# Performance work log

Measured on AMD Instinct MI355X. Metric: run time of the kernel, lower is better.

Reference implementation:

```python
import jax, jax.numpy as jnp
import numpy as np

EMBED = 256
HEADS = 8
B, T = 8, 1024


def setup_inputs() -> dict:
    key = jax.random.key(0)
    ks = jax.random.split(key, 6)
    scale = 1.0 / np.sqrt(EMBED)
    embeddings = jax.random.normal(ks[0], (B, T, EMBED), dtype=jnp.float32)
    # per-head full-width projections, stacked: [H, out=EMBED, in=EMBED] (torch Linear layout)
    Wq = jax.random.normal(ks[1], (HEADS, EMBED, EMBED), dtype=jnp.float32) * scale
    Wk = jax.random.normal(ks[2], (HEADS, EMBED, EMBED), dtype=jnp.float32) * scale
    Wv = jax.random.normal(ks[3], (HEADS, EMBED, EMBED), dtype=jnp.float32) * scale
    Wo = jax.random.normal(ks[4], (EMBED, HEADS * EMBED), dtype=jnp.float32) * (1.0 / np.sqrt(HEADS * EMBED))
    bo = jax.random.normal(ks[5], (EMBED,), dtype=jnp.float32) * 0.01
    return {"embeddings": embeddings, "Wq": Wq, "Wk": Wk, "Wv": Wv, "Wo": Wo, "bo": bo}


def reference(embeddings, Wq, Wk, Wv, Wo, bo):
    # x: [b,t,e]; W*: [h, out_e, in_e] (torch Linear: y = x @ W.T)
    q = jnp.einsum('bte,hde->hbtd', embeddings, Wq)
    k = jnp.einsum('bte,hde->hbtd', embeddings, Wk)
    v = jnp.einsum('bte,hde->hbtd', embeddings, Wv)
    # NOTE: original code has no 1/sqrt(d) scaling
    energy = jnp.einsum('hbid,hbjd->hbij', q, k)  # [h,b,t,t]
    t = embeddings.shape[1]
    causal = jnp.triu(jnp.ones((t, t), dtype=bool), k=1)
    energy = jnp.where(causal, -jnp.inf, energy)
    attn = jax.nn.softmax(energy, axis=-1)
    o = jnp.einsum('hbij,hbjd->hbid', attn, v)     # [h,b,t,e]
    b, _, _, e = o.shape[1], o.shape[0], o.shape[2], o.shape[3]
    o = jnp.transpose(o, (1, 2, 0, 3)).reshape(embeddings.shape[0], t, -1)  # [b,t,h*e]
    return o @ Wo.T + bo
```

## Files before the change

kernel.cpp:

```cpp
#include <hip/hip_runtime.h>
#include <hip/hip_bf16.h>

#define EMBED 256
#define HEADS 8
#define BATCH 8
#define SEQ   1024
#define NROWS 8192

typedef __attribute__((ext_vector_type(8))) _Float16 half8;
typedef __attribute__((ext_vector_type(4))) float f32x4;
typedef unsigned int  uint;
typedef unsigned short ushort;

#define QE   ((size_t)2097152)

__device__ __forceinline__ ushort f2h(float f) {
    union { _Float16 h; ushort u; } cv; cv.h = (_Float16)f; return cv.u;
}

__global__ __launch_bounds__(256) void convert_f16(
    const float* __restrict__ X,  const float* __restrict__ Wq,
    const float* __restrict__ Wk, const float* __restrict__ Wv,
    const float* __restrict__ Wo,
    ushort* __restrict__ Xf, ushort* __restrict__ Wqkf,
    ushort* __restrict__ Wvf, ushort* __restrict__ Wof)
{
    const int blk = blockIdx.x;
    const float* src; ushort* dst; int i;
    if (blk < 2048)      { src = X;  dst = Xf;            i = blk * 256 + threadIdx.x; }
    else if (blk < 2560) { src = Wq; dst = Wqkf;          i = (blk - 2048) * 256 + threadIdx.x; }
    else if (blk < 3072) { src = Wk; dst = Wqkf + 524288; i = (blk - 2560) * 256 + threadIdx.x; }
    else if (blk < 3584) { src = Wv; dst = Wvf;           i = (blk - 3072) * 256 + threadIdx.x; }
    else                 { src = Wo; dst = Wof;           i = (blk - 3584) * 256 + threadIdx.x; }
    const float4 v = ((const float4*)src)[i];
    uint2 P;
    P.x = (uint)f2h(v.x) | ((uint)f2h(v.y) << 16);
    P.y = (uint)f2h(v.z) | ((uint)f2h(v.w) << 16);
    ((uint2*)dst)[i] = P;
}

__device__ __forceinline__ void gemm1p_core(
    const ushort* __restrict__ Ag, const ushort* __restrict__ Bg,
    ushort* __restrict__ o0, ushort* __restrict__ o1,
    ushort* Ah, ushort* Bh, int wg, int Ntiles, int mode)
{
    const int m0 = (wg / Ntiles) * 128;
    const int n0 = (wg % Ntiles) * 128;

    const int tid = threadIdx.x, w = tid >> 6, l = tid & 63;
    const int wr = w >> 1, wc = w & 1, g = l >> 4, c16 = l & 15;
    const int sr = l >> 3, sb = l & 7;

    f32x4 acc[4][4];
#pragma unroll
    for (int mi = 0; mi < 4; ++mi)
#pragma unroll
        for (int ni = 0; ni < 4; ++ni) acc[mi][ni] = (f32x4){0.f, 0.f, 0.f, 0.f};

    for (int k0 = 0; k0 < 256; k0 += 64) {
        __syncthreads();
#pragma unroll
        for (int j = 0; j < 4; ++j) {
            const int rb = w * 32 + j * 8;
            const int r  = rb + sr;
            const size_t srcA = (size_t)(m0 + r) * 256 + k0 + ((sb ^ (r & 7)) * 8);
            __builtin_amdgcn_global_load_lds(Ag + srcA, &Ah[rb * 64], 16, 0, 0);
            const size_t srcB = (size_t)(n0 + r) * 256 + k0 + ((sb ^ (r & 7)) * 8);
            __builtin_amdgcn_global_load_lds(Bg + srcB, &Bh[rb * 64], 16, 0, 0);
        }
        asm volatile("s_waitcnt vmcnt(0)" ::: "memory");
        __syncthreads();

#pragma unroll
        for (int kh = 0; kh < 2; ++kh) {
            const int bsel = ((kh << 2) | g) ^ (c16 & 7);
            half8 af[4], bf[4];
#pragma unroll
            for (int mi = 0; mi < 4; ++mi)
                af[mi] = *(const half8*)&Ah[(wr * 64 + mi * 16 + c16) * 64 + bsel * 8];
#pragma unroll
            for (int ni = 0; ni < 4; ++ni)
                bf[ni] = *(const half8*)&Bh[(wc * 64 + ni * 16 + c16) * 64 + bsel * 8];
#pragma unroll
            for (int mi = 0; mi < 4; ++mi)
#pragma unroll
                for (int ni = 0; ni < 4; ++ni)
                    acc[mi][ni] = __builtin_amdgcn_mfma_f32_16x16x32_f16(af[mi], bf[ni], acc[mi][ni], 0, 0, 0);
        }
    }

#pragma unroll
    for (int mi = 0; mi < 4; ++mi)
#pragma unroll
        for (int ni = 0; ni < 4; ++ni) {
            const int n = n0 + wc * 64 + ni * 16 + c16;
            if (mode == 0) {
                const int op = n >> 11, hh = (n >> 8) & 7, d = n & 255;
                ushort* tq = (op ? o1 : o0) + (size_t)hh * QE + d;
#pragma unroll
                for (int j = 0; j < 4; ++j) {
                    const int m = m0 + wr * 64 + mi * 16 + 4 * g + j;
                    tq[(size_t)m * 256] = f2h(acc[mi][ni][j]);
                }
            } else {
#pragma unroll
                for (int j = 0; j < 4; ++j) {
                    const int m = m0 + wr * 64 + mi * 16 + 4 * g + j;
                    o0[(size_t)m * NROWS + n] = f2h(acc[mi][ni][j]);
                }
            }
        }
}

__global__ __launch_bounds__(256) void gemm_qkvt(
    const ushort* __restrict__ Xf,
    const ushort* __restrict__ Wqkf, const ushort* __restrict__ Wvf,
    ushort* __restrict__ qf, ushort* __restrict__ kf, ushort* __restrict__ vtb)
{
    __shared__ __align__(16) ushort Ah[128 * 64];
    __shared__ __align__(16) ushort Bh[128 * 64];
    const int bid = blockIdx.x;
    if (bid < 2048) {
        const int wg = (bid & 7) * 256 + (bid >> 3);
        gemm1p_core(Xf, Wqkf, qf, kf, Ah, Bh, wg, 32, 0);
    } else {
        const int b2 = bid - 2048;
        const int wg = (b2 & 7) * 128 + (b2 >> 3);
        gemm1p_core(Wvf, Xf, vtb, nullptr, Ah, Bh, wg, 64, 1);
    }
}

__global__ __launch_bounds__(256) void gemm_out_f16(
    const ushort* __restrict__ A, const ushort* __restrict__ Bw,
    const float* __restrict__ bias, float* __restrict__ fo)
{
    __shared__ __align__(16) ushort Ah[128 * 64];
    __shared__ __align__(16) ushort Bh[64 * 64];

    const int cpx = gridDim.x >> 3;
    const int wg  = (blockIdx.x & 7) * cpx + (blockIdx.x >> 3);
    const int m0 = (wg >> 2) * 128;
    const int n0 = (wg & 3) * 64;

    const int tid = threadIdx.x, w = tid >> 6, l = tid & 63;
    const int wr = w >> 1, wc = w & 1, g = l >> 4, c16 = l & 15;
    const int sr = l >> 3, sb = l & 7;

    f32x4 acc[4][2];
#pragma unroll
    for (int mi = 0; mi < 4; ++mi)
#pragma unroll
        for (int ni = 0; ni < 2; ++ni) acc[mi][ni] = (f32x4){0.f, 0.f, 0.f, 0.f};

    for (int k0 = 0; k0 < 2048; k0 += 64) {
        __syncthreads();
#pragma unroll
        for (int j = 0; j < 4; ++j) {
            const int rb = w * 32 + j * 8;
            const int r  = rb + sr;
            const size_t src = (size_t)(m0 + r) * 2048 + k0 + ((sb ^ (r & 7)) * 8);
            __builtin_amdgcn_global_load_lds(A + src, &Ah[rb * 64], 16, 0, 0);
        }
#pragma unroll
        for (int j = 0; j < 2; ++j) {
            const int rb = w * 16 + j * 8;
            const int r  = rb + sr;
            const size_t src = (size_t)(n0 + r) * 2048 + k0 + ((sb ^ (r & 7)) * 8);
            __builtin_amdgcn_global_load_lds(Bw + src, &Bh[rb * 64], 16, 0, 0);
        }
        asm volatile("s_waitcnt vmcnt(0)" ::: "memory");
        __syncthreads();

#pragma unroll
        for (int kh = 0; kh < 2; ++kh) {
            const int bsel = ((kh << 2) | g) ^ (c16 & 7);
            half8 af[4], bf[2];
#pragma unroll
            for (int mi = 0; mi < 4; ++mi)
                af[mi] = *(const half8*)&Ah[(wr * 64 + mi * 16 + c16) * 64 + bsel * 8];
#pragma unroll
            for (int ni = 0; ni < 2; ++ni)
                bf[ni] = *(const half8*)&Bh[(wc * 32 + ni * 16 + c16) * 64 + bsel * 8];
#pragma unroll
            for (int mi = 0; mi < 4; ++mi)
#pragma unroll
                for (int ni = 0; ni < 2; ++ni)
                    acc[mi][ni] = __builtin_amdgcn_mfma_f32_16x16x32_f16(af[mi], bf[ni], acc[mi][ni], 0, 0, 0);
        }
    }

#pragma unroll
    for (int mi = 0; mi < 4; ++mi)
#pragma unroll
        for (int ni = 0; ni < 2; ++ni) {
            const int n = n0 + wc * 32 + ni * 16 + c16;
            const float bb = bias[n];
#pragma unroll
            for (int j = 0; j < 4; ++j) {
                const int m = m0 + wr * 64 + mi * 16 + 4 * g + j;
                fo[(size_t)m * 256 + n] = acc[mi][ni][j] + bb;
            }
        }
}

__global__ __launch_bounds__(256, 3) void flash_mfma(
    const ushort* __restrict__ qf, const ushort* __restrict__ kf,
    const ushort* __restrict__ vt, ushort* __restrict__ ocf)
{
    __shared__ __align__(16) ushort Ks[2][32 * 256];
    __shared__ __align__(16) ushort VTs[256 * 32];
    __shared__ __align__(16) ushort Pls[4][512];

    const int bid = blockIdx.x;
    const int idx = bid >> 3;
    const int hb  = (bid & 7) * 8 + (idx & 7);
    const int qst = 15 - (idx >> 3);
    const int h = hb >> 3, b = hb & 7;

    const int tid = threadIdx.x;
    const int w = tid >> 6, l = tid & 63;
    const int g = l >> 4, c16 = l & 15;
    const size_t qk_base = (size_t)h * QE + (size_t)b * (SEQ * EMBED);
    const size_t vt_base = (size_t)h * QE + (size_t)b * SEQ;

    const int psw = (c16 >> 1) & 3;
    const int rsw = c16 & 7;
    const int qw0 = qst * 64 + w * 16;
    const int q0 = qw0 + c16;

    half8 qfr[8];
    {
        const ushort* qr = qf + qk_base + (size_t)q0 * EMBED + g * 8;
#pragma unroll
        for (int kc = 0; kc < 8; ++kc)
            qfr[kc] = *(const half8*)(qr + kc * 32);
    }

    const ushort* kbase = kf + qk_base;
    const ushort* vbase = vt + vt_base;
    const int krow_l = l >> 5, kblk = l & 31;
    const int vd_l = l >> 2,  vblk = l & 3;
    uint koff[4], voff[4];
#pragma unroll
    for (int j = 0; j < 4; ++j) {
        const int row = 8 * w + 2 * j + krow_l;
        koff[j] = (uint)(row * EMBED + ((kblk ^ (row & 7)) * 8));
        const int d = w * 64 + j * 16 + vd_l;
        const int phi = ((d >> 1) ^ (d >> 3)) & 3;
        voff[j] = (uint)(d * NROWS + ((vblk ^ phi) * 8));
    }

    f32x4 acc[16];
#pragma unroll
    for (int dt = 0; dt < 16; ++dt) acc[dt] = (f32x4){0.f, 0.f, 0.f, 0.f};
    float m_r = -1e30f, l_p = 0.f;

    char* pw = (char*)&Pls[w][0];
    const int nkt = 2 * qst + 2;

#pragma unroll
    for (int j = 0; j < 4; ++j)
        __builtin_amdgcn_global_load_lds(kbase + koff[j], &Ks[0][(8 * w + 2 * j) * 256], 16, 0, 0);
    asm volatile("s_waitcnt vmcnt(0)" ::: "memory");
    __syncthreads();

    for (int kt = 0; kt < nkt; ++kt) {
#pragma unroll
        for (int j = 0; j < 4; ++j)
            __builtin_amdgcn_global_load_lds(vbase + voff[j] + kt * 32,
                                             &VTs[(w * 64 + j * 16) * 32], 16, 0, 0);
        if (kt + 1 < nkt) {
            const ushort* kb = kbase + (size_t)(kt + 1) * (32 * EMBED);
#pragma unroll
            for (int j = 0; j < 4; ++j)
                __builtin_amdgcn_global_load_lds(kb + koff[j],
                                                 &Ks[(kt + 1) & 1][(8 * w + 2 * j) * 256], 16, 0, 0);
        }

        const bool active = (kt * 32 <= qw0 + 15);
        if (active) {
            const ushort* Kb = &Ks[kt & 1][0];
            f32x4 s0 = (f32x4){0.f, 0.f, 0.f, 0.f};
            f32x4 s1 = (f32x4){0.f, 0.f, 0.f, 0.f};
#pragma unroll
            for (int kc = 0; kc < 8; ++kc) {
                const int blk = ((kc * 4 + g) ^ rsw) * 8;
                const half8 a0 = *(const half8*)&Kb[c16 * 256 + blk];
                const half8 a1 = *(const half8*)&Kb[(c16 + 16) * 256 + blk];
                s0 = __builtin_amdgcn_mfma_f32_16x16x32_f16(a0, qfr[kc], s0, 0, 0, 0);
                s1 = __builtin_amdgcn_mfma_f32_16x16x32_f16(a1, qfr[kc], s1, 0, 0, 0);
            }
            const int k0b = kt * 32 + 4 * g;
            float p0[4], p1[4];
            float pm = -1e30f;
#pragma unroll
            for (int r = 0; r < 4; ++r) {
                p0[r] = (k0b + r      > q0) ? -1e30f : s0[r];
                p1[r] = (k0b + 16 + r > q0) ? -1e30f : s1[r];
                pm = fmaxf(pm, fmaxf(p0[r], p1[r]));
            }
            if (__any(pm > m_r + 8.f)) {
                float gm = fmaxf(pm, __shfl_xor(pm, 16));
                gm = fmaxf(gm, __shfl_xor(gm, 32));
                const float mn = fmaxf(m_r, gm);
                const float sc = __expf(m_r - mn);
                l_p *= sc;
#pragma unroll
                for (int dt = 0; dt < 16; ++dt) acc[dt] *= sc;
                m_r = mn;
            }
#pragma unroll
            for (int r = 0; r < 4; ++r) {
                p0[r] = __expf(p0[r] - m_r);
                p1[r] = __expf(p1[r] - m_r);
                l_p += p0[r] + p1[r];
            }
#pragma unroll
            for (int t = 0; t < 2; ++t)
#pragma unroll
                for (int u = 0; u < 2; ++u) {
                    const int kk = 16 * t + 4 * g + 2 * u;
                    const int off = c16 * 64 + (((kk >> 3) ^ psw) * 16) + (kk & 7) * 2;
                    const float lo = t ? p1[2 * u] : p0[2 * u];
                    const float hi = t ? p1[2 * u + 1] : p0[2 * u + 1];
                    *(uint*)(pw + off) = (uint)f2h(lo) | ((uint)f2h(hi) << 16);
                }
        }

        asm volatile("s_waitcnt vmcnt(0)" ::: "memory");
        __syncthreads();

        if (active) {
            const half8 pfrag = *(const half8*)(pw + c16 * 64 + ((g ^ psw) * 16));
#pragma unroll
            for (int dt = 0; dt < 16; ++dt) {
                const int d = dt * 16 + c16;
                const int phi = ((d >> 1) ^ (d >> 3)) & 3;
                const half8 va = *(const half8*)&VTs[d * 32 + ((g ^ phi) * 8)];
                acc[dt] = __builtin_amdgcn_mfma_f32_16x16x32_f16(va, pfrag, acc[dt], 0, 0, 0);
            }
        }
        __syncthreads();
    }

    l_p += __shfl_xor(l_p, 16);
    l_p += __shfl_xor(l_p, 32);
    const float inv = 1.f / l_p;
    ushort* orow = ocf + ((size_t)(b * SEQ) + q0) * (HEADS * EMBED) + h * EMBED;
#pragma unroll
    for (int dt = 0; dt < 16; ++dt) {
        const f32x4 o = acc[dt] * inv;
        uint2 P2;
        P2.x = (uint)f2h(o[0]) | ((uint)f2h(o[1]) << 16);
        P2.y = (uint)f2h(o[2]) | ((uint)f2h(o[3]) << 16);
        *(uint2*)(orow + dt * 16 + 4 * g) = P2;
    }
}

extern "C" void kernel_launch(void* const* d_in, const int* in_sizes, int n_in,
                              void* d_out, int out_size, void* d_ws, size_t ws_size,
                              hipStream_t stream) {
    const float* X  = (const float*)d_in[0];
    const float* Wq = (const float*)d_in[1];
    const float* Wk = (const float*)d_in[2];
    const float* Wv = (const float*)d_in[3];
    const float* Wo = (const float*)d_in[4];
    const float* bo = (const float*)d_in[5];

    ushort* ws16 = (ushort*)d_ws;
    ushort* qf   = ws16;
    ushort* kf   = ws16 +  8 * QE;
    ushort* vtb  = ws16 + 16 * QE;
    ushort* ocf  = ws16 + 24 * QE;
    ushort* ex   = ws16 + 32 * QE;
    ushort* Xf   = ex;
    ushort* Wqkf = ex + 2097152;
    ushort* Wvf  = ex + 2097152 + 1048576;
    ushort* Wof  = ex + 2097152 + 1048576 + 524288;
    float*  out  = (float*)d_out;

    convert_f16<<<4096, 256, 0, stream>>>(X, Wq, Wk, Wv, Wo, Xf, Wqkf, Wvf, Wof);

    gemm_qkvt<<<3072, 256, 0, stream>>>(Xf, Wqkf, Wvf, qf, kf, vtb);

    flash_mfma<<<1024, 256, 0, stream>>>(qf, kf, vtb, ocf);

    gemm_out_f16<<<256, 256, 0, stream>>>(ocf, Wof, bo, out);
}
```

Baseline: 141.4 us.

## Relax flash-attention barriers with partial vmcnt waits and halve out-GEMM M tile

In the attention kernel, __syncthreads is replaced by raw s_barrier plus sched_barrier. The wait before the P·V phase now uses vmcnt(4), so the prefetch of the next K tile can stay in flight while V is consumed, with a full wait moved to the end of the iteration. Separately, the output projection GEMM tile shrinks from 128 to 64 rows and launches 512 blocks instead of 256, to fill more CUs. Relying on vmcnt ordering and dropping the compiler's fence semantics risks LDS hazards if the load ordering assumptions are wrong.

```diff
diff --git a/kernel.cpp b/kernel.cpp
--- a/kernel.cpp
+++ b/kernel.cpp
@@ -134,39 +134,33 @@
     const ushort* __restrict__ A, const ushort* __restrict__ Bw,
     const float* __restrict__ bias, float* __restrict__ fo)
 {
-    __shared__ __align__(16) ushort Ah[128 * 64];
+    __shared__ __align__(16) ushort Ah[64 * 64];
     __shared__ __align__(16) ushort Bh[64 * 64];
 
-    const int cpx = gridDim.x >> 3;
-    const int wg  = (blockIdx.x & 7) * cpx + (blockIdx.x >> 3);
-    const int m0 = (wg >> 2) * 128;
+    const int wg = (blockIdx.x & 7) * 64 + (blockIdx.x >> 3);
+    const int m0 = (wg >> 2) * 64;
     const int n0 = (wg & 3) * 64;
 
     const int tid = threadIdx.x, w = tid >> 6, l = tid & 63;
     const int wr = w >> 1, wc = w & 1, g = l >> 4, c16 = l & 15;
     const int sr = l >> 3, sb = l & 7;
 
-    f32x4 acc[4][2];
-#pragma unroll
-    for (int mi = 0; mi < 4; ++mi)
+    f32x4 acc[2][2];
+#pragma unroll
+    for (int mi = 0; mi < 2; ++mi)
 #pragma unroll
         for (int ni = 0; ni < 2; ++ni) acc[mi][ni] = (f32x4){0.f, 0.f, 0.f, 0.f};
 
     for (int k0 = 0; k0 < 2048; k0 += 64) {
         __syncthreads();
-#pragma unroll
-        for (int j = 0; j < 4; ++j) {
-            const int rb = w * 32 + j * 8;
-            const int r  = rb + sr;
-            const size_t src = (size_t)(m0 + r) * 2048 + k0 + ((sb ^ (r & 7)) * 8);
-            __builtin_amdgcn_global_load_lds(A + src, &Ah[rb * 64], 16, 0, 0);
-        }
 #pragma unroll
         for (int j = 0; j < 2; ++j) {
             const int rb = w * 16 + j * 8;
             const int r  = rb + sr;
-            const size_t src = (size_t)(n0 + r) * 2048 + k0 + ((sb ^ (r & 7)) * 8);
-            __builtin_amdgcn_global_load_lds(Bw + src, &Bh[rb * 64], 16, 0, 0);
+            const size_t srcA = (size_t)(m0 + r) * 2048 + k0 + ((sb ^ (r & 7)) * 8);
+            __builtin_amdgcn_global_load_lds(A + srcA, &Ah[rb * 64], 16, 0, 0);
+            const size_t srcB = (size_t)(n0 + r) * 2048 + k0 + ((sb ^ (r & 7)) * 8);
+            __builtin_amdgcn_global_load_lds(Bw + srcB, &Bh[rb * 64], 16, 0, 0);
         }
         asm volatile("s_waitcnt vmcnt(0)" ::: "memory");
         __syncthreads();
@@ -174,15 +168,15 @@
 #pragma unroll
         for (int kh = 0; kh < 2; ++kh) {
             const int bsel = ((kh << 2) | g) ^ (c16 & 7);
-            half8 af[4], bf[2];
-#pragma unroll
-            for (int mi = 0; mi < 4; ++mi)
-                af[mi] = *(const half8*)&Ah[(wr * 64 + mi * 16 + c16) * 64 + bsel * 8];
+            half8 af[2], bf[2];
+#pragma unroll
+            for (int mi = 0; mi < 2; ++mi)
+                af[mi] = *(const half8*)&Ah[(wr * 32 + mi * 16 + c16) * 64 + bsel * 8];
 #pragma unroll
             for (int ni = 0; ni < 2; ++ni)
                 bf[ni] = *(const half8*)&Bh[(wc * 32 + ni * 16 + c16) * 64 + bsel * 8];
 #pragma unroll
-            for (int mi = 0; mi < 4; ++mi)
+            for (int mi = 0; mi < 2; ++mi)
 #pragma unroll
                 for (int ni = 0; ni < 2; ++ni)
                     acc[mi][ni] = __builtin_amdgcn_mfma_f32_16x16x32_f16(af[mi], bf[ni], acc[mi][ni], 0, 0, 0);
@@ -190,14 +184,14 @@
     }
 
 #pragma unroll
-    for (int mi = 0; mi < 4; ++mi)
+    for (int mi = 0; mi < 2; ++mi)
 #pragma unroll
         for (int ni = 0; ni < 2; ++ni) {
             const int n = n0 + wc * 32 + ni * 16 + c16;
             const float bb = bias[n];
 #pragma unroll
             for (int j = 0; j < 4; ++j) {
-                const int m = m0 + wr * 64 + mi * 16 + 4 * g + j;
+                const int m = m0 + wr * 32 + mi * 16 + 4 * g + j;
                 fo[(size_t)m * 256 + n] = acc[mi][ni][j] + bb;
             }
         }
@@ -262,14 +256,16 @@
     for (int j = 0; j < 4; ++j)
         __builtin_amdgcn_global_load_lds(kbase + koff[j], &Ks[0][(8 * w + 2 * j) * 256], 16, 0, 0);
     asm volatile("s_waitcnt vmcnt(0)" ::: "memory");
-    __syncthreads();
+    __builtin_amdgcn_s_barrier();
+    __builtin_amdgcn_sched_barrier(0);
 
     for (int kt = 0; kt < nkt; ++kt) {
 #pragma unroll
         for (int j = 0; j < 4; ++j)
             __builtin_amdgcn_global_load_lds(vbase + voff[j] + kt * 32,
                                              &VTs[(w * 64 + j * 16) * 32], 16, 0, 0);
-        if (kt + 1 < nkt) {
+        const bool havek = (kt + 1 < nkt);
+        if (havek) {
             const ushort* kb = kbase + (size_t)(kt + 1) * (32 * EMBED);
 #pragma unroll
             for (int j = 0; j < 4; ++j)
@@ -327,8 +323,10 @@
                 }
         }
 
-        asm volatile("s_waitcnt vmcnt(0)" ::: "memory");
-        __syncthreads();
+        if (havek) asm volatile("s_waitcnt vmcnt(4)" ::: "memory");
+        else       asm volatile("s_waitcnt vmcnt(0)" ::: "memory");
+        __builtin_amdgcn_s_barrier();
+        __builtin_amdgcn_sched_barrier(0);
 
         if (active) {
             const half8 pfrag = *(const half8*)(pw + c16 * 64 + ((g ^ psw) * 16));
@@ -340,7 +338,10 @@
                 acc[dt] = __builtin_amdgcn_mfma_f32_16x16x32_f16(va, pfrag, acc[dt], 0, 0, 0);
             }
         }
-        __syncthreads();
+
+        asm volatile("s_waitcnt vmcnt(0)" ::: "memory");
+        __builtin_amdgcn_s_barrier();
+        __builtin_amdgcn_sched_barrier(0);
     }
 
     l_p += __shfl_xor(l_p, 16);
@@ -385,5 +386,5 @@
 
     flash_mfma<<<1024, 256, 0, stream>>>(qf, kf, vtb, ocf);
 
-    gemm_out_f16<<<256, 256, 0, stream>>>(ocf, Wof, bo, out);
-}
+    gemm_out_f16<<<512, 256, 0, stream>>>(ocf, Wof, bo, out);
+}
```

After: 136.4 us. -3.5%, faster.
